# Kernel tuning notes

Hardware: AMD Instinct MI355X
Metric: run time of the kernel (lower is better)

## Reference

```python
import jax, jax.numpy as jnp
import numpy as np
from jax import lax

B, N, F, T = 16, 1024, 3, 12
K, C = 3, 64  # cheb order, num filters (chev == time filters == 64)
SC = 0.1      # init_scale


def setup_inputs() -> dict:
    key = jax.random.key(0)
    ks = jax.random.split(key, 20)
    rn = lambda k, shp: SC * jax.random.normal(k, shp, dtype=jnp.float32)
    inp = {
        'x': jax.random.normal(ks[0], (B, N, F, T), dtype=jnp.float32),
        # temporal attention params
        'U1': rn(ks[1], (N,)), 'U2': rn(ks[2], (F, N)), 'U3': rn(ks[3], (F,)),
        'b_e': rn(ks[4], (1, T, T)), 'V_e': rn(ks[5], (T, T)),
        # spatial attention params
        'W1': rn(ks[6], (T,)), 'W2': rn(ks[7], (F, T)), 'W3': rn(ks[8], (F,)),
        'b_s': rn(ks[9], (1, N, N)), 'V_s': rn(ks[10], (N, N)),
        # chebyshev polynomials T_0..T_{K-1} (dense (N,N) matrices) and Theta
        'cheb': jax.random.normal(ks[11], (K, N, N), dtype=jnp.float32) / np.sqrt(N),
        'Theta': rn(ks[12], (K, F, C)),
        # time conv (1,3) pad (0,1) and residual 1x1 conv
        'tc_w': rn(ks[13], (C, C, 1, 3)), 'tc_b': rn(ks[14], (C,)),
        'rc_w': rn(ks[15], (C, F, 1, 1)), 'rc_b': rn(ks[16], (C,)),
        # full-shape LayerNorm affine (normalized over the entire tensor)
        'ln_g': jnp.ones((B, N, C, T), dtype=jnp.float32),
        'ln_b': jnp.zeros((B, N, C, T), dtype=jnp.float32),
    }
    return inp


def _col_softmax(s):
    # softmax over axis 1, matching manual max-subtract/exp/sum in source
    s = s - s.max(axis=1, keepdims=True)
    e = jnp.exp(s)
    return e / e.sum(axis=1, keepdims=True)


def reference(x, U1, U2, U3, b_e, V_e, W1, W2, W3, b_s, V_s, cheb, Theta,
              tc_w, tc_b, rc_w, rc_b, ln_g, ln_b):
    # ---- temporal attention (B,T,T) ----
    lhs = jnp.einsum('bnft,n->btf', x, U1) @ U2            # (B,T,N)
    rhs = jnp.einsum('bnft,f->bnt', x, U3)                 # (B,N,T)
    sig = jax.nn.sigmoid(jnp.einsum('btn,bnu->btu', lhs, rhs) + b_e)
    e = jnp.einsum('bik,jk->bij', sig, V_e)                # V_e applied per source row
    temporal_at = _col_softmax(e)                          # (B,T,T)

    # x_tat = bmm(x.view(B,N*F,T), temporal_at)
    x_tat = jnp.einsum('bnft,btu->bnfu', x, temporal_at)   # (B,N,F,T)

    # ---- spatial attention (B,N,N) ----
    lhs2 = jnp.einsum('bnft,t->bnf', x_tat, W1) @ W2       # (B,N,T)
    rhs2 = jnp.einsum('bnft,f->btn', x_tat, W3)            # (B,T,N)
    sig2 = jax.nn.sigmoid(jnp.einsum('bnt,btm->bnm', lhs2, rhs2) + b_s)
    s = jnp.einsum('bik,jk->bij', sig2, V_s)
    sat = _col_softmax(s)                                  # (B,N,N)

    # ---- chebyshev conv with spatial attention, vectorized over K and T ----
    # out[b,m,c,t] = relu(sum_{k,n,f} T_k[n,m]*sat[b,n,m]*x[b,n,f,t]*Theta[k,f,c])
    Awt = cheb[None] * sat[:, None]                        # (B,K,N,N)
    rhs_c = jnp.einsum('bknm,bnft->bkmft', Awt, x)         # (B,K,N,F,T)
    gcn = jax.nn.relu(jnp.einsum('bkmft,kfc->bmct', rhs_c, Theta))  # (B,N,C,T)

    # ---- temporal conv (1,3) pad (0,1), operating on (B,C,N,T) ----
    dn = ('NCHW', 'OIHW', 'NCHW')
    tco = lax.conv_general_dilated(gcn.transpose(0, 2, 1, 3), tc_w, (1, 1),
                                   ((0, 0), (1, 1)), dimension_numbers=dn)
    tco = (tco + tc_b[None, :, None, None]).transpose(0, 2, 1, 3)  # (B,N,C,T)

    # ---- residual 1x1 conv (F==3 path) ----
    xres = lax.conv_general_dilated(x.transpose(0, 2, 1, 3), rc_w, (1, 1),
                                    ((0, 0), (0, 0)), dimension_numbers=dn)
    xres = (xres + rc_b[None, :, None, None]).transpose(0, 2, 1, 3)

    # ---- relu + LayerNorm over the entire (B,N,C,T) tensor ----
    y = jax.nn.relu(xres + tco)
    mu = y.mean()
    var = jnp.mean((y - mu) ** 2)
    return (y - mu) * lax.rsqrt(var + 1e-5) * ln_g + ln_b
```

## Files before the change

kernel.cpp:

```cpp
#include <hip/hip_runtime.h>
#include <hip/hip_bf16.h>
#include <math.h>

#define BB 16
#define NN_ 1024
#define TT 12

typedef __attribute__((ext_vector_type(8))) short bf16x8;
typedef __attribute__((ext_vector_type(4))) float f32x4;

static const size_t ACC_OFF    = 0;
static const size_t COLSUM_OFF = 16;
static const size_t TAT_OFF    = 16400;
static const size_t LHST_OFF   = 18704;
static const size_t RHS2_OFF   = 215312;
static const size_t VSB_OFF    = 411920;
static const size_t SIG2B_OFF  = 936208;
static const size_t CHEBB_OFF  = 9324816;
static const size_t EXPS_OFF   = 10897680;
static const size_t RHSC_OFF   = 19286288;
static const size_t WTG_OFF    = 26364176;
static const size_t PART_OFF   = 26370320;

#define RHSC_SZ 1769472

__device__ __forceinline__ float wave_reduce_sum(float v) {
    #pragma unroll
    for (int off = 32; off > 0; off >>= 1) v += __shfl_down(v, off);
    return v;
}

__device__ __forceinline__ unsigned short f2b(float f) {
    __hip_bfloat16 h = __float2bfloat16(f);
    return *(unsigned short*)&h;
}
__device__ __forceinline__ float b2f(unsigned short u) {
    return __uint_as_float(((unsigned int)u) << 16);
}

__global__ void k_init(float* __restrict__ ws) {
    int i = blockIdx.x * 256 + threadIdx.x;
    if (i < 16400) ws[i] = 0.f;
}

__global__ __launch_bounds__(256) void k_cvtw(
    const float* __restrict__ tcw, unsigned short* __restrict__ WtG)
{
    for (int j = threadIdx.x; j < 12288; j += 256) {
        const int row = j >> 6;
        const int cp  = j & 63;
        const int d   = row >> 6;
        const int c   = row & 63;
        WtG[j] = f2b(tcw[c * 192 + 3 * cp + d]);
    }
}

__global__ __launch_bounds__(256) void k_temporal(
    const float* __restrict__ x, const float* __restrict__ U1,
    const float* __restrict__ U2, const float* __restrict__ U3,
    const float* __restrict__ be, const float* __restrict__ Ve,
    float* __restrict__ tat)
{
    const int b = blockIdx.x;
    const int tid = threadIdx.x;
    const int wid = tid >> 6, lane = tid & 63;
    float lA[36], lM[36];
    #pragma unroll
    for (int i = 0; i < 36; ++i) { lA[i] = 0.f; lM[i] = 0.f; }
    const float u30 = U3[0], u31 = U3[1], u32 = U3[2];
    for (int n = tid; n < NN_; n += 256) {
        const float* xp = x + ((size_t)b * NN_ + n) * 36;
        float xr[36];
        #pragma unroll
        for (int i = 0; i < 9; ++i) *(float4*)&xr[i*4] = *(const float4*)(xp + i*4);
        const float u1  = U1[n];
        const float u20 = U2[n], u21 = U2[NN_ + n], u22 = U2[2*NN_ + n];
        #pragma unroll
        for (int t = 0; t < 12; ++t) {
            float ru = xr[t]*u30 + xr[12+t]*u31 + xr[24+t]*u32;
            lM[t]    += u20 * ru;
            lM[12+t] += u21 * ru;
            lM[24+t] += u22 * ru;
            lA[t]    += xr[t]    * u1;
            lA[12+t] += xr[12+t] * u1;
            lA[24+t] += xr[24+t] * u1;
        }
    }
    __shared__ float pA[4][36], pM[4][36];
    __shared__ float tA[36], tM[36], sgs[144], es[144], cmax[12], csum[12];
    #pragma unroll
    for (int i = 0; i < 36; ++i) {
        float v = wave_reduce_sum(lA[i]);
        if (lane == 0) pA[wid][i] = v;
        float w = wave_reduce_sum(lM[i]);
        if (lane == 0) pM[wid][i] = w;
    }
    __syncthreads();
    if (tid < 36) tA[tid] = pA[0][tid] + pA[1][tid] + pA[2][tid] + pA[3][tid];
    else if (tid < 72) {
        int i = tid - 36;
        tM[i] = pM[0][i] + pM[1][i] + pM[2][i] + pM[3][i];
    }
    __syncthreads();
    if (tid < 144) {
        int t = tid / 12, u = tid % 12;
        float p = tA[t]*tM[u] + tA[12+t]*tM[12+u] + tA[24+t]*tM[24+u];
        p += be[tid];
        sgs[tid] = 1.f / (1.f + expf(-p));
    }
    __syncthreads();
    if (tid < 144) {
        int i = tid / 12, j = tid % 12;
        float e = 0.f;
        #pragma unroll
        for (int k = 0; k < 12; ++k) e += sgs[i*12 + k] * Ve[j*12 + k];
        es[tid] = e;
    }
    __syncthreads();
    if (tid < 12) {
        int j = tid;
        float m = -1e30f;
        for (int i = 0; i < 12; ++i) m = fmaxf(m, es[i*12 + j]);
        float sx = 0.f;
        for (int i = 0; i < 12; ++i) sx += expf(es[i*12 + j] - m);
        cmax[j] = m; csum[j] = sx;
    }
    __syncthreads();
    if (tid < 144) {
        int j = tid % 12;
        tat[(size_t)b*144 + tid] = expf(es[tid] - cmax[j]) / csum[j];
    }
}

__global__ __launch_bounds__(256) void k_xtat(
    const float* __restrict__ x, const float* __restrict__ tat,
    const float* __restrict__ W1, const float* __restrict__ W2,
    const float* __restrict__ W3,
    float* __restrict__ lhsT, float* __restrict__ rhs2)
{
    const int id = blockIdx.x * 256 + threadIdx.x;
    const int b = id >> 10, n = id & 1023;
    const float* xp = x + (size_t)id * 36;
    float xr[36];
    #pragma unroll
    for (int i = 0; i < 9; ++i) *(float4*)&xr[i*4] = *(const float4*)(xp + i*4);
    const float* tp = tat + (size_t)b * 144;
    float xt[36];
    #pragma unroll
    for (int f = 0; f < 3; ++f)
        #pragma unroll
        for (int u = 0; u < 12; ++u) {
            float s = 0.f;
            #pragma unroll
            for (int t = 0; t < 12; ++t) s += xr[f*12 + t] * tp[t*12 + u];
            xt[f*12 + u] = s;
        }
    float lA0 = 0.f, lA1 = 0.f, lA2 = 0.f;
    #pragma unroll
    for (int t = 0; t < 12; ++t) {
        float w = W1[t];
        lA0 += xt[t]*w; lA1 += xt[12+t]*w; lA2 += xt[24+t]*w;
    }
    #pragma unroll
    for (int t2 = 0; t2 < 12; ++t2)
        lhsT[(size_t)id*12 + t2] = lA0*W2[t2] + lA1*W2[12+t2] + lA2*W2[24+t2];
    const float w30 = W3[0], w31 = W3[1], w32 = W3[2];
    #pragma unroll
    for (int u = 0; u < 12; ++u)
        rhs2[((size_t)b*12 + u)*NN_ + n] = xt[u]*w30 + xt[12+u]*w31 + xt[24+u]*w32;
}

__global__ __launch_bounds__(256) void k_sig2(
    const float* __restrict__ lhsT, const float* __restrict__ rhs2,
    const float* __restrict__ bs, __hip_bfloat16* __restrict__ sig2b)
{
    const unsigned int idx = blockIdx.x * 256u + threadIdx.x;
    const int m = (int)(idx & 1023u);
    const unsigned int bn = idx >> 10;
    const int b = (int)(bn >> 10);
    const int n = (int)(bn & 1023u);
    const float* lp = lhsT + (size_t)bn * 12;
    const float* rp = rhs2 + (size_t)b * 12 * NN_ + m;
    float z = bs[(size_t)n * NN_ + m];
    #pragma unroll
    for (int t = 0; t < 12; ++t) z += lp[t] * rp[(size_t)t * NN_];
    sig2b[idx] = __float2bfloat16(1.f / (1.f + __expf(-z)));
}

__global__ __launch_bounds__(256) void k_cvt4(
    const float* __restrict__ src, unsigned short* __restrict__ dst)
{
    const int i = blockIdx.x * 256 + threadIdx.x;
    float4 v = ((const float4*)src)[i];
    ushort4 o;
    o.x = f2b(v.x); o.y = f2b(v.y); o.z = f2b(v.z); o.w = f2b(v.w);
    ((ushort4*)dst)[i] = o;
}

__global__ __launch_bounds__(256) void k_gemm_s_mfma(
    const short* __restrict__ A, const short* __restrict__ Bm,
    unsigned short* __restrict__ E, float* __restrict__ colsum)
{
    __shared__ short As[128 * 32];
    __shared__ short Bs[128 * 32];
    __shared__ unsigned short Es[64][136];
    const int b  = blockIdx.z;
    const int i0 = blockIdx.y * 128;
    const int j0 = blockIdx.x * 128;
    const int tid = threadIdx.x;
    const int wid = tid >> 6;
    const int lane = tid & 63;
    const int wr = wid & 1, wc = wid >> 1;
    const short* Ab = A + (size_t)b * NN_ * NN_;

    f32x4 acc[4][4];
    const f32x4 z4 = {0.f, 0.f, 0.f, 0.f};
    #pragma unroll
    for (int m = 0; m < 4; ++m)
        #pragma unroll
        for (int n = 0; n < 4; ++n) acc[m][n] = z4;

    const int srow = lane >> 2;
    const int schk = lane & 3;
    const int fr = lane & 15;
    const int kb = (lane >> 4) * 8;

    for (int k0 = 0; k0 < NN_; k0 += 32) {
        #pragma unroll
        for (int q = 0; q < 2; ++q) {
            const int rb = (wid * 2 + q) * 16;
            const short* srcA = Ab + (size_t)(i0 + rb + srow) * NN_ + k0 + schk * 8;
            const short* srcB = Bm + (size_t)(j0 + rb + srow) * NN_ + k0 + schk * 8;
            __builtin_amdgcn_global_load_lds(
                (const __attribute__((address_space(1))) unsigned int*)srcA,
                (__attribute__((address_space(3))) unsigned int*)(As + rb * 32), 16, 0, 0);
            __builtin_amdgcn_global_load_lds(
                (const __attribute__((address_space(1))) unsigned int*)srcB,
                (__attribute__((address_space(3))) unsigned int*)(Bs + rb * 32), 16, 0, 0);
        }
        __syncthreads();
        bf16x8 aF[4], bF[4];
        #pragma unroll
        for (int m = 0; m < 4; ++m)
            aF[m] = *(const bf16x8*)(As + (wr*64 + m*16 + fr) * 32 + kb);
        #pragma unroll
        for (int n = 0; n < 4; ++n)
            bF[n] = *(const bf16x8*)(Bs + (wc*64 + n*16 + fr) * 32 + kb);
        #pragma unroll
        for (int m = 0; m < 4; ++m)
            #pragma unroll
            for (int n = 0; n < 4; ++n)
                acc[m][n] = __builtin_amdgcn_mfma_f32_16x16x32_bf16(aF[m], bF[n], acc[m][n], 0, 0, 0);
        __syncthreads();
    }
    unsigned short* Ep = E + (size_t)b * NN_ * NN_;
    const int cn = lane & 15;
    const int r0 = (lane >> 4) * 4;
    float cs[4] = {0.f, 0.f, 0.f, 0.f};
    #pragma unroll
    for (int half = 0; half < 2; ++half) {
        if (wr == half) {
            #pragma unroll
            for (int m = 0; m < 4; ++m)
                #pragma unroll
                for (int n = 0; n < 4; ++n)
                    #pragma unroll
                    for (int r = 0; r < 4; ++r) {
                        float e = __expf(acc[m][n][r]);
                        Es[m*16 + r0 + r][wc*64 + n*16 + cn] = f2b(e);
                        cs[n] += e;
                    }
        }
        __syncthreads();
        #pragma unroll
        for (int it = 0; it < 4; ++it) {
            const int idx = it * 256 + tid;
            const int rL = idx >> 4;
            const int cq = idx & 15;
            const int4 v = *(const int4*)&Es[rL][cq * 8];
            *(int4*)(Ep + (size_t)(i0 + half*64 + rL) * NN_ + j0 + cq * 8) = v;
        }
        __syncthreads();
    }
    #pragma unroll
    for (int n = 0; n < 4; ++n) {
        float s = cs[n];
        s += __shfl_xor(s, 16);
        s += __shfl_xor(s, 32);
        if (lane < 16)
            atomicAdd(&colsum[b * NN_ + j0 + wc*64 + n*16 + cn], s);
    }
}

#define XSS 48
__global__ __launch_bounds__(256) void k_rhsc(
    const unsigned short* __restrict__ chebb, const unsigned short* __restrict__ expS,
    const float* __restrict__ colsum, const float* __restrict__ x,
    float* __restrict__ rhsc)
{
    __shared__ float w[3 * 16 * 64];
    __shared__ float xs[16 * XSS];
    __shared__ float red[256 * 9];
    const int m0 = blockIdx.x * 64;
    const int b  = blockIdx.y;
    const int z  = blockIdx.z;
    const int nbase = z * 512;
    const int tid = threadIdx.x;
    const int usplit = tid >> 6;
    const int lane = tid & 63;
    const int mg = lane >> 2;
    const int q  = lane & 3;
    const int nn  = tid >> 4;
    const int mm  = (tid & 15) << 2;
    float rcs[4];
    {
        const float* cp = colsum + b * NN_ + m0 + mm;
        rcs[0] = 1.f / cp[0]; rcs[1] = 1.f / cp[1];
        rcs[2] = 1.f / cp[2]; rcs[3] = 1.f / cp[3];
    }
    int xlds[3], xsrc[3];
    bool xok[3];
    #pragma unroll
    for (int j = 0; j < 3; ++j) {
        const int idx = tid + j * 256;
        xok[j] = idx < 576;
        const int n2 = idx / 36, jj = idx - n2 * 36;
        const int sec = jj / 9, off = jj - sec * 9;
        xlds[j] = n2 * XSS + sec * 12 + off;
        xsrc[j] = n2 * 36 + jj;
    }

    float acc[3][4][9];
    #pragma unroll
    for (int k = 0; k < 3; ++k)
        #pragma unroll
        for (int mi = 0; mi < 4; ++mi)
            #pragma unroll
            for (int jj = 0; jj < 9; ++jj) acc[k][mi][jj] = 0.f;

    const unsigned short* sb = expS + (size_t)b * NN_ * NN_;
    const float* xb = x + (size_t)b * NN_ * 36;
    const size_t rowoff = (size_t)nn * NN_ + m0 + mm;

    ushort4 ps, pc0, pc1, pc2;
    float px[3];
    {
        const size_t r = (size_t)nbase * NN_ + rowoff;
        ps  = *(const ushort4*)(sb + r);
        pc0 = *(const ushort4*)(chebb + r);
        pc1 = *(const ushort4*)(chebb + (size_t)NN_ * NN_ + r);
        pc2 = *(const ushort4*)(chebb + (size_t)2 * NN_ * NN_ + r);
        #pragma unroll
        for (int j = 0; j < 3; ++j)
            if (xok[j]) px[j] = xb[(size_t)nbase * 36 + xsrc[j]];
    }

    for (int s = 0; s < 32; ++s) {
        {
            const float st0 = b2f(ps.x) * rcs[0], st1 = b2f(ps.y) * rcs[1];
            const float st2 = b2f(ps.z) * rcs[2], st3 = b2f(ps.w) * rcs[3];
            float4 w0, w1, w2;
            w0.x = b2f(pc0.x)*st0; w0.y = b2f(pc0.y)*st1; w0.z = b2f(pc0.z)*st2; w0.w = b2f(pc0.w)*st3;
            w1.x = b2f(pc1.x)*st0; w1.y = b2f(pc1.y)*st1; w1.z = b2f(pc1.z)*st2; w1.w = b2f(pc1.w)*st3;
            w2.x = b2f(pc2.x)*st0; w2.y = b2f(pc2.y)*st1; w2.z = b2f(pc2.z)*st2; w2.w = b2f(pc2.w)*st3;
            *(float4*)&w[(0 * 16 + nn) * 64 + mm] = w0;
            *(float4*)&w[(1 * 16 + nn) * 64 + mm] = w1;
            *(float4*)&w[(2 * 16 + nn) * 64 + mm] = w2;
            #pragma unroll
            for (int j = 0; j < 3; ++j)
                if (xok[j]) xs[xlds[j]] = px[j];
        }
        __syncthreads();
        if (s + 1 < 32) {
            const int n1 = nbase + (s + 1) * 16;
            const size_t r = (size_t)n1 * NN_ + rowoff;
            ps  = *(const ushort4*)(sb + r);
            pc0 = *(const ushort4*)(chebb + r);
            pc1 = *(const ushort4*)(chebb + (size_t)NN_ * NN_ + r);
            pc2 = *(const ushort4*)(chebb + (size_t)2 * NN_ * NN_ + r);
            #pragma unroll
            for (int j = 0; j < 3; ++j)
                if (xok[j]) px[j] = xb[(size_t)n1 * 36 + xsrc[j]];
        }
        #pragma unroll
        for (int ui = 0; ui < 4; ++ui) {
            const int u = usplit * 4 + ui;
            float xv[9];
            *(float4*)&xv[0] = *(const float4*)&xs[u * XSS + q * 12];
            *(float4*)&xv[4] = *(const float4*)&xs[u * XSS + q * 12 + 4];
            xv[8] = xs[u * XSS + q * 12 + 8];
            float wv[3][4];
            #pragma unroll
            for (int k = 0; k < 3; ++k)
                *(float4*)&wv[k][0] = *(const float4*)&w[(k * 16 + u) * 64 + mg * 4];
            #pragma unroll
            for (int k = 0; k < 3; ++k)
                #pragma unroll
                for (int mi = 0; mi < 4; ++mi) {
                    const float wk = wv[k][mi];
                    #pragma unroll
                    for (int jj = 0; jj < 9; ++jj)
                        acc[k][mi][jj] += wk * xv[jj];
                }
        }
        __syncthreads();
    }

    float* outb = rhsc + (size_t)z * RHSC_SZ;
    #pragma unroll
    for (int r = 0; r < 12; ++r) {
        const int k = r >> 2, mi = r & 3;
        #pragma unroll
        for (int jj = 0; jj < 9; ++jj) red[tid * 9 + jj] = acc[k][mi][jj];
        __syncthreads();
        if (usplit == 0) {
            float s[9];
            #pragma unroll
            for (int jj = 0; jj < 9; ++jj)
                s[jj] = red[lane * 9 + jj] + red[(64 + lane) * 9 + jj]
                      + red[(128 + lane) * 9 + jj] + red[(192 + lane) * 9 + jj];
            float* rp = outb + (((size_t)b * 3 + k) * NN_ + m0 + mg * 4 + mi) * 36 + q * 9;
            #pragma unroll
            for (int jj = 0; jj < 9; ++jj) rp[jj] = s[jj];
        }
        __syncthreads();
    }
}

#define G2S 72
#define RSTR 112
__global__ __launch_bounds__(256) void k_y7(
    const float* __restrict__ rhsc,
    const unsigned short* __restrict__ WtG,
    const float* __restrict__ Theta, const float* __restrict__ x,
    const float* __restrict__ tcb,
    const float* __restrict__ rcw, const float* __restrict__ rcb,
    float* __restrict__ y, float* __restrict__ partials)
{
    __shared__ unsigned short Gs2[193 * G2S];
    __shared__ float Rs[16 * RSTR];
    __shared__ float xls[16 * 36];
    __shared__ float red[8];
    const int tid = threadIdx.x;
    const int wid = tid >> 6, lane = tid & 63;
    const int blk = blockIdx.x;

    const int bb = (blk * 16) >> 10;
    const int nb = (blk * 16) & 1023;
    for (int idx = tid; idx < 432; idx += 256) {
        const int i = idx / 27;
        const int r = idx - i * 27;
        const int k = r / 9;
        const int q = r - k * 9;
        const size_t off = (((size_t)bb * 3 + k) * NN_ + nb + i) * 36 + q * 4;
        float4 a = *(const float4*)(rhsc + off);
        float4 b = *(const float4*)(rhsc + RHSC_SZ + off);
        a.x += b.x; a.y += b.y; a.z += b.z; a.w += b.w;
        *(float4*)&Rs[i * RSTR + k * 36 + q * 4] = a;
    }
    if (tid < 36) ((unsigned int*)(Gs2 + 192 * G2S))[tid] = 0u;
    if (tid < 144)
        ((float4*)xls)[tid] = ((const float4*)(x + (size_t)blk * 16 * 36))[tid];
    __syncthreads();

    {
        float th[9];
        #pragma unroll
        for (int j = 0; j < 9; ++j) th[j] = Theta[j * 64 + lane];
        #pragma unroll
        for (int ii = 0; ii < 4; ++ii) {
            const int i = wid * 4 + ii;
            float g[12];
            #pragma unroll
            for (int t = 0; t < 12; ++t) g[t] = 0.f;
            #pragma unroll
            for (int kf = 0; kf < 9; ++kf) {
                const float* rp = Rs + i * RSTR + kf * 12;
                float4 v0 = *(const float4*)(rp);
                float4 v1 = *(const float4*)(rp + 4);
                float4 v2 = *(const float4*)(rp + 8);
                const float w = th[kf];
                g[0] += v0.x*w; g[1] += v0.y*w; g[2]  += v0.z*w; g[3]  += v0.w*w;
                g[4] += v1.x*w; g[5] += v1.y*w; g[6]  += v1.z*w; g[7]  += v1.w*w;
                g[8] += v2.x*w; g[9] += v2.y*w; g[10] += v2.z*w; g[11] += v2.w*w;
            }
            #pragma unroll
            for (int t = 0; t < 12; ++t)
                Gs2[(i*12 + t) * G2S + lane] = f2b(fmaxf(g[t], 0.f));
        }
    }
    __syncthreads();

    const int cl = lane & 15, kg = lane >> 4;
    bf16x8 aW[3][2];
    #pragma unroll
    for (int d = 0; d < 3; ++d)
        #pragma unroll
        for (int kb = 0; kb < 2; ++kb)
            aW[d][kb] = *(const bf16x8*)(WtG + (d*64 + wid*16 + cl) * 64 + kb*32 + kg*8);
    float tb[4], rb[4], rw0[4], rw1[4], rw2[4];
    #pragma unroll
    for (int r = 0; r < 4; ++r) {
        const int c = wid*16 + kg*4 + r;
        tb[r] = tcb[c]; rb[r] = rcb[c];
        rw0[r] = rcw[c*3]; rw1[r] = rcw[c*3+1]; rw2[r] = rcw[c*3+2];
    }
    float ls = 0.f, lss = 0.f;
    #pragma unroll
    for (int ct = 0; ct < 12; ++ct) {
        const int nt = ct * 16 + cl;
        const int i = nt / 12;
        const int t = nt - i * 12;
        const unsigned short* g1 = Gs2 + nt * G2S + kg * 8;
        const unsigned short* g0 = (t == 0)  ? (Gs2 + 192 * G2S + kg * 8) : (g1 - G2S);
        const unsigned short* g2 = (t == 11) ? (Gs2 + 192 * G2S + kg * 8) : (g1 + G2S);
        f32x4 a4 = {0.f, 0.f, 0.f, 0.f};
        #pragma unroll
        for (int kb = 0; kb < 2; ++kb) {
            a4 = __builtin_amdgcn_mfma_f32_16x16x32_bf16(aW[0][kb], *(const bf16x8*)(g0 + kb*32), a4, 0, 0, 0);
            a4 = __builtin_amdgcn_mfma_f32_16x16x32_bf16(aW[1][kb], *(const bf16x8*)(g1 + kb*32), a4, 0, 0, 0);
            a4 = __builtin_amdgcn_mfma_f32_16x16x32_bf16(aW[2][kb], *(const bf16x8*)(g2 + kb*32), a4, 0, 0, 0);
        }
        const float x0 = xls[i*36 + t];
        const float x1 = xls[i*36 + 12 + t];
        const float x2 = xls[i*36 + 24 + t];
        float* yp = y + (size_t)(blk*16 + i) * 768 + (wid*16 + kg*4) * 12 + t;
        #pragma unroll
        for (int r = 0; r < 4; ++r) {
            const float xres = rb[r] + x0*rw0[r] + x1*rw1[r] + x2*rw2[r];
            const float v = fmaxf(xres + a4[r] + tb[r], 0.f);
            ls += v; lss += v * v;
            yp[r * 12] = v;
        }
    }
    ls  = wave_reduce_sum(ls);
    lss = wave_reduce_sum(lss);
    if (lane == 0) { red[wid] = ls; red[4 + wid] = lss; }
    __syncthreads();
    if (tid == 0) {
        partials[blk]        = red[0] + red[1] + red[2] + red[3];
        partials[1024 + blk] = red[4] + red[5] + red[6] + red[7];
    }
}

__global__ __launch_bounds__(256) void k_fin2(
    const float* __restrict__ partials, float* __restrict__ acc)
{
    const int tid = threadIdx.x;
    const int wid = tid >> 6, lane = tid & 63;
    float s = 0.f, ss = 0.f;
    #pragma unroll
    for (int j = tid; j < 1024; j += 256) {
        s  += partials[j];
        ss += partials[1024 + j];
    }
    s  = wave_reduce_sum(s);
    ss = wave_reduce_sum(ss);
    __shared__ float rs[4], rss[4];
    if (lane == 0) { rs[wid] = s; rss[wid] = ss; }
    __syncthreads();
    if (tid == 0) {
        const float cnt = (float)((size_t)BB * NN_ * 64 * TT);
        float tot  = rs[0] + rs[1] + rs[2] + rs[3];
        float tots = rss[0] + rss[1] + rss[2] + rss[3];
        float mu = tot / cnt;
        float var = tots / cnt - mu * mu;
        acc[2] = mu;
        acc[3] = rsqrtf(var + 1e-5f);
    }
}

__global__ __launch_bounds__(256) void k_norm(
    float* __restrict__ y, const float* __restrict__ lng,
    const float* __restrict__ lnb, const float* __restrict__ acc)
{
    const unsigned int i = blockIdx.x * 256u + threadIdx.x;
    const float mu = acc[2], inv = acc[3];
    float4 v  = ((const float4*)y)[i];
    float4 gv = ((const float4*)lng)[i];
    float4 bv = ((const float4*)lnb)[i];
    v.x = (v.x - mu) * inv * gv.x + bv.x;
    v.y = (v.y - mu) * inv * gv.y + bv.y;
    v.z = (v.z - mu) * inv * gv.z + bv.z;
    v.w = (v.w - mu) * inv * gv.w + bv.w;
    ((float4*)y)[i] = v;
}

extern "C" void kernel_launch(void* const* d_in, const int* in_sizes, int n_in,
                              void* d_out, int out_size, void* d_ws, size_t ws_size,
                              hipStream_t stream)
{
    const float* x    = (const float*)d_in[0];
    const float* U1   = (const float*)d_in[1];
    const float* U2   = (const float*)d_in[2];
    const float* U3   = (const float*)d_in[3];
    const float* be   = (const float*)d_in[4];
    const float* Ve   = (const float*)d_in[5];
    const float* W1   = (const float*)d_in[6];
    const float* W2   = (const float*)d_in[7];
    const float* W3   = (const float*)d_in[8];
    const float* bs   = (const float*)d_in[9];
    const float* Vs   = (const float*)d_in[10];
    const float* cheb = (const float*)d_in[11];
    const float* Th   = (const float*)d_in[12];
    const float* tcw  = (const float*)d_in[13];
    const float* tcb  = (const float*)d_in[14];
    const float* rcw  = (const float*)d_in[15];
    const float* rcb  = (const float*)d_in[16];
    const float* lng  = (const float*)d_in[17];
    const float* lnb  = (const float*)d_in[18];
    float* out = (float*)d_out;
    float* ws  = (float*)d_ws;

    float* acc    = ws + ACC_OFF;
    float* colsum = ws + COLSUM_OFF;
    float* tat    = ws + TAT_OFF;
    float* lhsT   = ws + LHST_OFF;
    float* rhs2   = ws + RHS2_OFF;
    unsigned short* Vsb   = (unsigned short*)(ws + VSB_OFF);
    unsigned short* sig2b = (unsigned short*)(ws + SIG2B_OFF);
    unsigned short* chebb = (unsigned short*)(ws + CHEBB_OFF);
    unsigned short* expS  = (unsigned short*)(ws + EXPS_OFF);
    float* rhsc   = ws + RHSC_OFF;
    unsigned short* WtG   = (unsigned short*)(ws + WTG_OFF);
    float* partials = ws + PART_OFF;

    k_init<<<65, 256, 0, stream>>>(ws);
    k_cvtw<<<1, 256, 0, stream>>>(tcw, WtG);
    k_temporal<<<BB, 256, 0, stream>>>(x, U1, U2, U3, be, Ve, tat);
    k_xtat<<<(BB * NN_) / 256, 256, 0, stream>>>(x, tat, W1, W2, W3, lhsT, rhs2);
    k_cvt4<<<(NN_ * NN_) / 1024, 256, 0, stream>>>(Vs, Vsb);
    k_cvt4<<<(3 * NN_ * NN_) / 1024, 256, 0, stream>>>(cheb, chebb);
    k_sig2<<<(BB * NN_ * NN_) / 256, 256, 0, stream>>>(lhsT, rhs2, bs, (__hip_bfloat16*)sig2b);
    k_gemm_s_mfma<<<dim3(8, 8, BB), 256, 0, stream>>>((const short*)sig2b, (const short*)Vsb, expS, colsum);
    k_rhsc<<<dim3(16, BB, 2), 256, 0, stream>>>(chebb, expS, colsum, x, rhsc);
    k_y7<<<(BB * NN_) / 16, 256, 0, stream>>>(rhsc, WtG, Th, x, tcb, rcw, rcb, out, partials);
    k_fin2<<<1, 256, 0, stream>>>(partials, acc);
    k_norm<<<(BB * NN_ * 64 * TT) / 4 / 256, 256, 0, stream>>>(out, lng, lnb, acc);
}
```

Measured before the change: 409.9 us.

## Rewrite rhsc contraction with bf16 MFMA instead of scalar FMA

Replaces the fp32 scalar outer-product accumulation in k_rhsc with bf16 16x16x32 MFMA instructions. The attention-weighted Chebyshev tiles and x are staged in shared memory as bf16 with transposed layouts. The cross-wave reduction through shared memory is removed because each wave now owns 16 output rows. It drops the register prefetch double-buffering and rounds the products and x to bf16 before accumulation, which costs precision.

```diff
diff --git a/kernel.cpp b/kernel.cpp
--- a/kernel.cpp
+++ b/kernel.cpp
@@ -292,138 +292,103 @@
     }
 }
 
-#define XSS 48
+#define AWS 40
 __global__ __launch_bounds__(256) void k_rhsc(
     const unsigned short* __restrict__ chebb, const unsigned short* __restrict__ expS,
     const float* __restrict__ colsum, const float* __restrict__ x,
     float* __restrict__ rhsc)
 {
-    __shared__ float w[3 * 16 * 64];
-    __shared__ float xs[16 * XSS];
-    __shared__ float red[256 * 9];
+    __shared__ __align__(16) unsigned short awt[3][64][AWS];
+    __shared__ __align__(16) unsigned short xts[48][AWS];
     const int m0 = blockIdx.x * 64;
     const int b  = blockIdx.y;
     const int z  = blockIdx.z;
     const int nbase = z * 512;
     const int tid = threadIdx.x;
-    const int usplit = tid >> 6;
-    const int lane = tid & 63;
-    const int mg = lane >> 2;
-    const int q  = lane & 3;
-    const int nn  = tid >> 4;
-    const int mm  = (tid & 15) << 2;
-    float rcs[4];
+    const int w = tid >> 6, lane = tid & 63;
+    const int sn  = tid >> 4;
+    const int sm4 = (tid & 15) * 4;
+    float rcs4[4];
     {
-        const float* cp = colsum + b * NN_ + m0 + mm;
-        rcs[0] = 1.f / cp[0]; rcs[1] = 1.f / cp[1];
-        rcs[2] = 1.f / cp[2]; rcs[3] = 1.f / cp[3];
-    }
-    int xlds[3], xsrc[3];
-    bool xok[3];
-    #pragma unroll
-    for (int j = 0; j < 3; ++j) {
-        const int idx = tid + j * 256;
-        xok[j] = idx < 576;
-        const int n2 = idx / 36, jj = idx - n2 * 36;
-        const int sec = jj / 9, off = jj - sec * 9;
-        xlds[j] = n2 * XSS + sec * 12 + off;
-        xsrc[j] = n2 * 36 + jj;
-    }
-
-    float acc[3][4][9];
+        float4 rv = *(const float4*)(colsum + b * NN_ + m0 + sm4);
+        rcs4[0] = 1.f / rv.x; rcs4[1] = 1.f / rv.y;
+        rcs4[2] = 1.f / rv.z; rcs4[3] = 1.f / rv.w;
+    }
+    for (int i = tid; i < 12 * AWS; i += 256) xts[36 + i / AWS][i % AWS] = 0;
+
+    const int fr  = lane & 15;
+    const int kb8 = (lane >> 4) * 8;
+
+    f32x4 acc[3][3];
+    const f32x4 z4 = {0.f, 0.f, 0.f, 0.f};
     #pragma unroll
     for (int k = 0; k < 3; ++k)
         #pragma unroll
-        for (int mi = 0; mi < 4; ++mi)
-            #pragma unroll
-            for (int jj = 0; jj < 9; ++jj) acc[k][mi][jj] = 0.f;
+        for (int t = 0; t < 3; ++t) acc[k][t] = z4;
 
     const unsigned short* sb = expS + (size_t)b * NN_ * NN_;
     const float* xb = x + (size_t)b * NN_ * 36;
-    const size_t rowoff = (size_t)nn * NN_ + m0 + mm;
-
-    ushort4 ps, pc0, pc1, pc2;
-    float px[3];
-    {
-        const size_t r = (size_t)nbase * NN_ + rowoff;
-        ps  = *(const ushort4*)(sb + r);
-        pc0 = *(const ushort4*)(chebb + r);
-        pc1 = *(const ushort4*)(chebb + (size_t)NN_ * NN_ + r);
-        pc2 = *(const ushort4*)(chebb + (size_t)2 * NN_ * NN_ + r);
-        #pragma unroll
-        for (int j = 0; j < 3; ++j)
-            if (xok[j]) px[j] = xb[(size_t)nbase * 36 + xsrc[j]];
-    }
-
-    for (int s = 0; s < 32; ++s) {
-        {
-            const float st0 = b2f(ps.x) * rcs[0], st1 = b2f(ps.y) * rcs[1];
-            const float st2 = b2f(ps.z) * rcs[2], st3 = b2f(ps.w) * rcs[3];
-            float4 w0, w1, w2;
-            w0.x = b2f(pc0.x)*st0; w0.y = b2f(pc0.y)*st1; w0.z = b2f(pc0.z)*st2; w0.w = b2f(pc0.w)*st3;
-            w1.x = b2f(pc1.x)*st0; w1.y = b2f(pc1.y)*st1; w1.z = b2f(pc1.z)*st2; w1.w = b2f(pc1.w)*st3;
-            w2.x = b2f(pc2.x)*st0; w2.y = b2f(pc2.y)*st1; w2.z = b2f(pc2.z)*st2; w2.w = b2f(pc2.w)*st3;
-            *(float4*)&w[(0 * 16 + nn) * 64 + mm] = w0;
-            *(float4*)&w[(1 * 16 + nn) * 64 + mm] = w1;
-            *(float4*)&w[(2 * 16 + nn) * 64 + mm] = w2;
-            #pragma unroll
-            for (int j = 0; j < 3; ++j)
-                if (xok[j]) xs[xlds[j]] = px[j];
+
+    for (int s = 0; s < 16; ++s) {
+        const int n0 = nbase + s * 32;
+        #pragma unroll
+        for (int sl = 0; sl < 2; ++sl) {
+            const int n = sn + sl * 16;
+            const size_t r = (size_t)(n0 + n) * NN_ + m0 + sm4;
+            ushort4 pe = *(const ushort4*)(sb + r);
+            const float e0 = b2f(pe.x) * rcs4[0], e1 = b2f(pe.y) * rcs4[1];
+            const float e2 = b2f(pe.z) * rcs4[2], e3 = b2f(pe.w) * rcs4[3];
+            #pragma unroll
+            for (int k = 0; k < 3; ++k) {
+                ushort4 pc = *(const ushort4*)(chebb + (size_t)k * NN_ * NN_ + r);
+                awt[k][sm4 + 0][n] = f2b(b2f(pc.x) * e0);
+                awt[k][sm4 + 1][n] = f2b(b2f(pc.y) * e1);
+                awt[k][sm4 + 2][n] = f2b(b2f(pc.z) * e2);
+                awt[k][sm4 + 3][n] = f2b(b2f(pc.w) * e3);
+            }
+        }
+        #pragma unroll
+        for (int j = 0; j < 2; ++j) {
+            const int c2 = tid + 256 * j;
+            if (c2 < 288) {
+                const int n2 = c2 / 9, fq = c2 - n2 * 9;
+                float4 xv = *(const float4*)(xb + (size_t)(n0 + n2) * 36 + fq * 4);
+                xts[fq * 4 + 0][n2] = f2b(xv.x);
+                xts[fq * 4 + 1][n2] = f2b(xv.y);
+                xts[fq * 4 + 2][n2] = f2b(xv.z);
+                xts[fq * 4 + 3][n2] = f2b(xv.w);
+            }
         }
         __syncthreads();
-        if (s + 1 < 32) {
-            const int n1 = nbase + (s + 1) * 16;
-            const size_t r = (size_t)n1 * NN_ + rowoff;
-            ps  = *(const ushort4*)(sb + r);
-            pc0 = *(const ushort4*)(chebb + r);
-            pc1 = *(const ushort4*)(chebb + (size_t)NN_ * NN_ + r);
-            pc2 = *(const ushort4*)(chebb + (size_t)2 * NN_ * NN_ + r);
-            #pragma unroll
-            for (int j = 0; j < 3; ++j)
-                if (xok[j]) px[j] = xb[(size_t)n1 * 36 + xsrc[j]];
-        }
-        #pragma unroll
-        for (int ui = 0; ui < 4; ++ui) {
-            const int u = usplit * 4 + ui;
-            float xv[9];
-            *(float4*)&xv[0] = *(const float4*)&xs[u * XSS + q * 12];
-            *(float4*)&xv[4] = *(const float4*)&xs[u * XSS + q * 12 + 4];
-            xv[8] = xs[u * XSS + q * 12 + 8];
-            float wv[3][4];
-            #pragma unroll
-            for (int k = 0; k < 3; ++k)
-                *(float4*)&wv[k][0] = *(const float4*)&w[(k * 16 + u) * 64 + mg * 4];
-            #pragma unroll
-            for (int k = 0; k < 3; ++k)
+        bf16x8 aF[3], bF[3];
+        #pragma unroll
+        for (int k = 0; k < 3; ++k)
+            aF[k] = *(const bf16x8*)(&awt[k][w * 16 + fr][kb8]);
+        #pragma unroll
+        for (int t = 0; t < 3; ++t)
+            bF[t] = *(const bf16x8*)(&xts[t * 16 + fr][kb8]);
+        #pragma unroll
+        for (int k = 0; k < 3; ++k)
+            #pragma unroll
+            for (int t = 0; t < 3; ++t)
+                acc[k][t] = __builtin_amdgcn_mfma_f32_16x16x32_bf16(aF[k], bF[t], acc[k][t], 0, 0, 0);
+        __syncthreads();
+    }
+
+    float* outb = rhsc + (size_t)z * RHSC_SZ;
+    const int orow = (lane >> 4) * 4;
+    #pragma unroll
+    for (int k = 0; k < 3; ++k) {
+        const size_t rowbase = (size_t)(b * 3 + k) * NN_ + m0 + w * 16 + orow;
+        #pragma unroll
+        for (int t = 0; t < 3; ++t) {
+            const int col = t * 16 + fr;
+            if (col < 36) {
                 #pragma unroll
-                for (int mi = 0; mi < 4; ++mi) {
-                    const float wk = wv[k][mi];
-                    #pragma unroll
-                    for (int jj = 0; jj < 9; ++jj)
-                        acc[k][mi][jj] += wk * xv[jj];
-                }
-        }
-        __syncthreads();
-    }
-
-    float* outb = rhsc + (size_t)z * RHSC_SZ;
-    #pragma unroll
-    for (int r = 0; r < 12; ++r) {
-        const int k = r >> 2, mi = r & 3;
-        #pragma unroll
-        for (int jj = 0; jj < 9; ++jj) red[tid * 9 + jj] = acc[k][mi][jj];
-        __syncthreads();
-        if (usplit == 0) {
-            float s[9];
-            #pragma unroll
-            for (int jj = 0; jj < 9; ++jj)
-                s[jj] = red[lane * 9 + jj] + red[(64 + lane) * 9 + jj]
-                      + red[(128 + lane) * 9 + jj] + red[(192 + lane) * 9 + jj];
-            float* rp = outb + (((size_t)b * 3 + k) * NN_ + m0 + mg * 4 + mi) * 36 + q * 9;
-            #pragma unroll
-            for (int jj = 0; jj < 9; ++jj) rp[jj] = s[jj];
-        }
-        __syncthreads();
+                for (int r = 0; r < 4; ++r)
+                    outb[(rowbase + r) * 36 + col] = acc[k][t][r];
+            }
+        }
     }
 }
 
```

After: 397.4 us. 3.1% less time.
